# Performance work log

Hardware: AMD Instinct MI355X
Metric: run time of the kernel (lower is better)

## Reference

```python
import jax, jax.numpy as jnp
import numpy as np

EMB = 64
NODE_DIM = 5
T = 5
B, N = 8, 512


def setup_inputs() -> dict:
    key = jax.random.key(0)
    ks = jax.random.split(key, 24)
    def w(k, shape):
        return jax.random.normal(k, shape, dtype=jnp.float32) * 0.1
    xv = jax.random.normal(ks[0], (B, N, NODE_DIM), dtype=jnp.float32)
    Ws = jax.random.uniform(ks[1], (B, N, N), dtype=jnp.float32)
    reach = jax.random.bernoulli(ks[2], 0.5, (B, N))
    reach = reach.at[:, 0].set(True)  # guarantee at least one reachable node
    return {
        'xv': xv, 'Ws': Ws, 'reachable_nodes': reach,
        'W1a': w(ks[3], (NODE_DIM, EMB)), 'b1a': w(ks[4], (EMB,)),
        'W1b': w(ks[5], (EMB, EMB)),      'b1b': w(ks[6], (EMB,)),
        'W2':  w(ks[7], (EMB, EMB)),      'b2':  w(ks[8], (EMB,)),
        'W3':  w(ks[9], (EMB, EMB)),      'b3':  w(ks[10], (EMB,)),
        'w4':  w(ks[11], (EMB,)),         'b4':  w(ks[12], (EMB,)),
        'W6':  w(ks[13], (EMB, EMB)),     'b6':  w(ks[14], (EMB,)),
        'W7':  w(ks[15], (EMB, EMB)),     'b7':  w(ks[16], (EMB,)),
        'W51': w(ks[17], (2 * EMB, EMB)), 'b51': w(ks[18], (EMB,)),
        'w52': w(ks[19], (EMB,)),         'b52': w(ks[20], ()),
    }


def _struc2vec(xv, Ws, W1a, b1a, W1b, b1b, W2, b2, W3, b3, w4, b4):
    # s1: per-node feature embedding [B,N,E]
    s1 = jax.nn.relu(xv @ W1a + b1a) @ W1b + b1b
    # edge-feature path: relu(theta4(Ws[...,None])) summed over dim 1 -> [B,N,E]
    s3_1 = jax.nn.relu(Ws[..., None] * w4 + b4)  # [B,N,N,E]
    s3 = jnp.sum(s3_1, axis=1) @ W3 + b3         # [B,N,E]
    mu = jnp.zeros(s1.shape, dtype=s1.dtype)
    for _ in range(T):
        s2 = jnp.einsum('bnm,bme->bne', Ws, mu) @ W2 + b2
        mu = jax.nn.relu(s1 + s2 + s3)
    return mu


def reference(xv, Ws, reachable_nodes, W1a, b1a, W1b, b1b, W2, b2, W3, b3,
              w4, b4, W6, b6, W7, b7, W51, b51, w52, b52):
    mu = _struc2vec(xv, Ws, W1a, b1a, W1b, b1b, W2, b2, W3, b3, w4, b4)
    # global state broadcast to every node + local per-node action embedding
    global_state = jnp.sum(mu, axis=1, keepdims=True) @ W6 + b6  # [B,1,E]
    global_state = jnp.broadcast_to(global_state, mu.shape)      # [B,N,E]
    local_action = mu @ W7 + b7                                  # [B,N,E]
    rep = jax.nn.relu(jnp.concatenate([global_state, local_action], axis=2))
    rep = jax.nn.relu(rep) @ W51 + b51                           # relu(relu(.)) as in source
    prob_logits = rep @ w52 + b52                                # [B,N]
    prob_logits = jnp.where(reachable_nodes, prob_logits, -jnp.inf)
    return prob_logits
```

## Files before the change

### kernel.cpp

```cpp
#include <hip/hip_runtime.h>
#include <hip/hip_bf16.h>
#include <cstdint>
#include <cstddef>

#define BB 8
#define NN 512
#define EE 64

typedef __attribute__((ext_vector_type(8))) short short8v;
typedef __attribute__((ext_vector_type(4))) float f32x4;
typedef __attribute__((ext_vector_type(2))) float f32x2;
typedef __attribute__((ext_vector_type(4))) unsigned int u32x4;
typedef __attribute__((ext_vector_type(2))) unsigned int u32x2;

static __device__ __forceinline__ unsigned short f2bf(float f) {
  __hip_bfloat16 h = __float2bfloat16(f);
  return *reinterpret_cast<unsigned short*>(&h);
}
static __device__ __forceinline__ float bf2f(unsigned short u) {
  unsigned x = ((unsigned)u) << 16;
  float f; __builtin_memcpy(&f, &x, 4); return f;
}
static __device__ __forceinline__ u32x4 ld_b128_sc(const void* p) {
  u32x4 v;
  asm volatile("global_load_dwordx4 %0, %1, off sc0 sc1"
               : "=v"(v) : "v"(p) : "memory");
  return v;
}
static __device__ __forceinline__ unsigned ld_b32_sc(const void* p) {
  unsigned v;
  asm volatile("global_load_dword %0, %1, off sc0 sc1\n\ts_waitcnt vmcnt(0)"
               : "=v"(v) : "v"(p) : "memory");
  return v;
}
static __device__ __forceinline__ void st_b64_sc(void* p, u32x2 v) {
  asm volatile("global_store_dwordx2 %0, %1, off sc0 sc1"
               :: "v"(p), "v"(v) : "memory");
}
static __device__ __forceinline__ void st_b32_sc(void* p, unsigned v) {
  asm volatile("global_store_dword %0, %1, off sc0 sc1"
               :: "v"(p), "v"(v) : "memory");
}
static __device__ __forceinline__ void vm0() {
  asm volatile("s_waitcnt vmcnt(0)" ::: "memory");
}

__global__ __launch_bounds__(512) void k_fused(
    const float* __restrict__ Ws, const float* __restrict__ xv,
    const float* __restrict__ W1a, const float* __restrict__ b1a,
    const float* __restrict__ W1b, const float* __restrict__ b1b,
    const float* __restrict__ W2, const float* __restrict__ b2,
    const float* __restrict__ W3, const float* __restrict__ b3,
    const float* __restrict__ w4, const float* __restrict__ b4,
    const float* __restrict__ W6, const float* __restrict__ b6,
    const float* __restrict__ W7, const float* __restrict__ b7,
    const float* __restrict__ W51, const float* __restrict__ b51,
    const float* __restrict__ w52, const float* __restrict__ b52,
    const void* __restrict__ reach, float* __restrict__ out,
    unsigned short* __restrict__ z0, unsigned short* __restrict__ z1,
    unsigned short* __restrict__ z2, unsigned short* __restrict__ z3,
    float* __restrict__ gpart, unsigned* __restrict__ flags) {
  const int blk = blockIdx.x;
  const int b = (blk >> 3) & 7;
  const int stripe = ((blk & 7) << 2) | (blk >> 6);
  const int n0 = stripe << 4;
  const int t = threadIdx.x;
  const int w = t >> 6, l = t & 63, lr = l & 15, hi = l >> 4;
  const int lk = hi * 8, nq = hi * 4, eb = w & 3, kh = w >> 2;

  __shared__ __attribute__((aligned(16))) float tileT[16][132];
  __shared__ float sp[16][68];
  __shared__ float half_[16][68];
  __shared__ float hh[16][68];
  __shared__ float base_lds[16][68];
  __shared__ float yred[16][68];
  __shared__ __attribute__((aligned(16))) unsigned short muzA[512];
  __shared__ __attribute__((aligned(16))) unsigned short muzB[512];
  __shared__ float gsl[64], gsr[64], v7l[64], w52l[64], pl_lds[16];
  __shared__ float g0c;
  __shared__ int sbig, sflt;

  auto arrive = [&](int idx) {
    vm0();
    __syncthreads();
    if (t == 0) st_b32_sc(&flags[(b * 8 + idx) * 32 + stripe], 1u);
  };
  auto wait = [&](int idx) {
    if (t < 64) {
      const unsigned* fp = &flags[(b * 8 + idx) * 32 + (t & 31)];
      while (true) {
        unsigned v = ld_b32_sc(fp);
        if (__ballot(v != 0u) == ~0ull) break;
        __builtin_amdgcn_s_sleep(1);
      }
    }
    __syncthreads();
  };

  auto muz_store = [&](int node, int e, float v) {
    int eh = e & 31;
    unsigned short* dst = (e < 32) ? muzA : muzB;
    dst[((eh >> 3) * 16 + node) * 8 + (eh & 7)] = f2bf(v);
  };

  const float* wsbase = Ws + (size_t)b * NN * NN;
  const int lrow = t >> 2, lc4 = (t & 3) * 4;
  float4 tr0 = *(const float4*)&wsbase[(size_t)(0 * 128 + lrow) * NN + n0 + lc4];
  float4 tr1 = *(const float4*)&wsbase[(size_t)(1 * 128 + lrow) * NN + n0 + lc4];
  float4 tr2 = *(const float4*)&wsbase[(size_t)(2 * 128 + lrow) * NN + n0 + lc4];
  float4 tr3 = *(const float4*)&wsbase[(size_t)(3 * 128 + lrow) * NN + n0 + lc4];

  short8v WBa = {}, WBb = {};
  if (w < 4) {
    union { unsigned short u[8]; short8v v; } pa, pb;
#pragma unroll
    for (int j = 0; j < 8; ++j) {
      pa.u[j] = f2bf(W2[(8 * hi + j) * EE + 16 * w + lr]);
      pb.u[j] = f2bf(W2[(8 * hi + j + 32) * EE + 16 * w + lr]);
    }
    WBa = pa.v; WBb = pb.v;
  }

  {
    int e = t & 63;
#pragma unroll
    for (int p = 0; p < 2; ++p) {
      int rr = p * 8 + (t >> 6);
      const float* x = xv + ((size_t)b * NN + n0 + rr) * 5;
      float h = b1a[e];
      h = fmaf(x[0], W1a[0 * EE + e], h);
      h = fmaf(x[1], W1a[1 * EE + e], h);
      h = fmaf(x[2], W1a[2 * EE + e], h);
      h = fmaf(x[3], W1a[3 * EE + e], h);
      h = fmaf(x[4], W1a[4 * EE + e], h);
      hh[rr][e] = fmaxf(h, 0.f);
    }
  }
  {
    int ih = t >> 8;
    int n = (t >> 4) & 15;
    int e0 = (t & 15) * 4;
    float4 w4v = *(const float4*)&w4[e0];
    float4 b4v = *(const float4*)&b4[e0];
    f32x2 w4lo = {w4v.x, w4v.y}, w4hi_ = {w4v.z, w4v.w};
    f32x2 b4lo = {b4v.x, b4v.y}, b4hi_ = {b4v.z, b4v.w};
    f32x2 acclo = {0.f, 0.f}, acchi = {0.f, 0.f};
    const f32x2 zz = {0.f, 0.f};
    int ib = ih * 64;
#pragma unroll
    for (int c = 0; c < 4; ++c) {
      float4 tv = (c == 0) ? tr0 : (c == 1) ? tr1 : (c == 2) ? tr2 : tr3;
      tileT[lc4 + 0][lrow] = tv.x;
      tileT[lc4 + 1][lrow] = tv.y;
      tileT[lc4 + 2][lrow] = tv.z;
      tileT[lc4 + 3][lrow] = tv.w;
      __syncthreads();
#pragma unroll
      for (int i4 = 0; i4 < 16; ++i4) {
        float4 wv = *(const float4*)&tileT[n][ib + i4 * 4];
#pragma unroll
        for (int k = 0; k < 4; ++k) {
          float ww = (k == 0) ? wv.x : (k == 1) ? wv.y : (k == 2) ? wv.z : wv.w;
          f32x2 wp = {ww, ww};
          acclo += __builtin_elementwise_max(
              __builtin_elementwise_fma(wp, w4lo, b4lo), zz);
          acchi += __builtin_elementwise_max(
              __builtin_elementwise_fma(wp, w4hi_, b4hi_), zz);
        }
      }
      __syncthreads();
    }
    if (ih) {
      half_[n][e0] = acclo.x; half_[n][e0 + 1] = acclo.y;
      half_[n][e0 + 2] = acchi.x; half_[n][e0 + 3] = acchi.y;
    }
    __syncthreads();
    if (!ih) {
      sp[n][e0]     = acclo.x + half_[n][e0];
      sp[n][e0 + 1] = acclo.y + half_[n][e0 + 1];
      sp[n][e0 + 2] = acchi.x + half_[n][e0 + 2];
      sp[n][e0 + 3] = acchi.y + half_[n][e0 + 3];
    }
  }
  __syncthreads();
  {
    int e = t & 63;
#pragma unroll
    for (int p = 0; p < 2; ++p) {
      int rr = p * 8 + (t >> 6);
      float s = b1b[e] + b3[e] + b2[e];
#pragma unroll 8
      for (int j = 0; j < EE; ++j)
        s = fmaf(hh[rr][j], W1b[j * EE + e], fmaf(sp[rr][j], W3[j * EE + e], s));
      base_lds[rr][e] = s;
      muz_store(rr, e, fmaxf(s, 0.f));
    }
  }
  __syncthreads();

  auto zphase = [&](unsigned short* dst) {
    if (w < 4) {
      short8v a0 = *(const short8v*)&muzA[l * 8];
      short8v a1 = *(const short8v*)&muzB[l * 8];
      f32x4 zacc = {0.f, 0.f, 0.f, 0.f};
      zacc = __builtin_amdgcn_mfma_f32_16x16x32_bf16(a0, WBa, zacc, 0, 0, 0);
      zacc = __builtin_amdgcn_mfma_f32_16x16x32_bf16(a1, WBb, zacc, 0, 0, 0);
      ushort4 u;
      u.x = f2bf(zacc[0]); u.y = f2bf(zacc[1]);
      u.z = f2bf(zacc[2]); u.w = f2bf(zacc[3]);
      u32x2 v; __builtin_memcpy(&v, &u, 8);
      st_b64_sc(dst + ((size_t)b * EE + 16 * w + lr) * NN + n0 + 4 * hi, v);
    }
  };

  zphase(z0);
  arrive(0);

  short8v A0, A1, A2, A3, A4, A5, A6, A7;
  {
    const float* arow = wsbase + (size_t)(n0 + lr) * NN + kh * 256 + lk;
    union { unsigned short u[8]; short8v v; } pk;
#define LDA(DST, OFF)                                                        \
    { float4 fa = *(const float4*)(arow + OFF);                              \
      float4 fb = *(const float4*)(arow + OFF + 4);                          \
      pk.u[0] = f2bf(fa.x); pk.u[1] = f2bf(fa.y);                            \
      pk.u[2] = f2bf(fa.z); pk.u[3] = f2bf(fa.w);                            \
      pk.u[4] = f2bf(fb.x); pk.u[5] = f2bf(fb.y);                            \
      pk.u[6] = f2bf(fb.z); pk.u[7] = f2bf(fb.w);                            \
      DST = pk.v; }
    LDA(A0, 0)   LDA(A1, 32)  LDA(A2, 64)  LDA(A3, 96)
    LDA(A4, 128) LDA(A5, 160) LDA(A6, 192) LDA(A7, 224)
#undef LDA
  }

  auto prop = [&](const unsigned short* zsrc) {
    const unsigned short* Bp =
        zsrc + ((size_t)b * EE + eb * 16 + lr) * NN + kh * 256 + lk;
    short8v q0 = *(const short8v*)(Bp + 0);
    short8v q1 = *(const short8v*)(Bp + 32);
    short8v q2 = *(const short8v*)(Bp + 64);
    short8v q3 = *(const short8v*)(Bp + 96);
    short8v q4 = *(const short8v*)(Bp + 128);
    short8v q5 = *(const short8v*)(Bp + 160);
    short8v q6 = *(const short8v*)(Bp + 192);
    short8v q7 = *(const short8v*)(Bp + 224);
    f32x4 acc = {0.f, 0.f, 0.f, 0.f};
    acc = __builtin_amdgcn_mfma_f32_16x16x32_bf16(A0, q0, acc, 0, 0, 0);
    acc = __builtin_amdgcn_mfma_f32_16x16x32_bf16(A1, q1, acc, 0, 0, 0);
    acc = __builtin_amdgcn_mfma_f32_16x16x32_bf16(A2, q2, acc, 0, 0, 0);
    acc = __builtin_amdgcn_mfma_f32_16x16x32_bf16(A3, q3, acc, 0, 0, 0);
    acc = __builtin_amdgcn_mfma_f32_16x16x32_bf16(A4, q4, acc, 0, 0, 0);
    acc = __builtin_amdgcn_mfma_f32_16x16x32_bf16(A5, q5, acc, 0, 0, 0);
    acc = __builtin_amdgcn_mfma_f32_16x16x32_bf16(A6, q6, acc, 0, 0, 0);
    acc = __builtin_amdgcn_mfma_f32_16x16x32_bf16(A7, q7, acc, 0, 0, 0);
    if (kh == 1) {
#pragma unroll
      for (int q = 0; q < 4; ++q) yred[nq + q][eb * 16 + lr] = acc[q];
    }
    __syncthreads();
    if (kh == 0) {
      int ep = eb * 16 + lr;
#pragma unroll
      for (int q = 0; q < 4; ++q) {
        float v = fmaxf(base_lds[nq + q][ep] + acc[q] + yred[nq + q][ep], 0.f);
        muz_store(nq + q, ep, v);
      }
    }
    __syncthreads();
  };

  wait(0);
  prop(z0); zphase(z1); arrive(1); wait(1);
  prop(z1); zphase(z2); arrive(2); wait(2);
  prop(z2); zphase(z3); arrive(3); wait(3);
  prop(z3);

  if (t < 64) {
    int eh = t & 31, jj = t & 7, lb = (eh >> 3) * 16;
    const unsigned short* dst = (t < 32) ? muzA : muzB;
    float s = 0.f;
#pragma unroll
    for (int n = 0; n < 16; ++n) s += bf2f(dst[(lb + n) * 8 + jj]);
    st_b32_sc(&gpart[((size_t)b * 32 + stripe) * EE + t], __float_as_uint(s));
  }
  arrive(4);

  if (t == 0) { sbig = 0; sflt = 0; }
  if (t < 64) w52l[t] = w52[t];
  __syncthreads();
  if (t < 256) {
    const unsigned int* rw = (const unsigned int*)reach;
    bool big = false, flt = false;
#pragma unroll
    for (int l2 = 0; l2 < 4; ++l2) {
      unsigned int v = rw[t + l2 * 256];
      if (v > 1u) big = true;
      if (v == 0x3f800000u) flt = true;
    }
    if (big) sbig = 1;
    if (flt) sflt = 1;
  }
  if (t >= 320 && t < 384) {
    int j = t - 320;
    float v = 0.f;
#pragma unroll 8
    for (int e = 0; e < EE; ++e) v = fmaf(W51[(EE + j) * EE + e], w52[e], v);
    v7l[j] = v;
  }
  __syncthreads();
#pragma unroll
  for (int p = 0; p < 2; ++p) {
    int n = p * 8 + (t >> 6), e7 = t & 63;
    float la = b7[e7];
#pragma unroll
    for (int h = 0; h < 2; ++h) {
      const unsigned short* dst = h ? muzB : muzA;
#pragma unroll
      for (int h2 = 0; h2 < 4; ++h2) {
        short8v mv = *(const short8v*)&dst[(h2 * 16 + n) * 8];
#pragma unroll
        for (int j = 0; j < 8; ++j)
          la = fmaf(bf2f((unsigned short)mv[j]),
                    W7[(h * 32 + h2 * 8 + j) * EE + e7], la);
      }
    }
    float c = fmaxf(la, 0.f) * v7l[e7];
#pragma unroll
    for (int off = 32; off > 0; off >>= 1) c += __shfl_down(c, off, 64);
    if (e7 == 0) pl_lds[n] = c;
  }

  wait(4);

  float* gacc = &tileT[0][0];
  {
    int s = t >> 4, e4 = (t & 15) * 4;
    u32x4 v = ld_b128_sc(&gpart[((size_t)b * 32 + s) * EE + e4]);
    vm0();
    gacc[s * EE + e4 + 0] = __uint_as_float(v.x);
    gacc[s * EE + e4 + 1] = __uint_as_float(v.y);
    gacc[s * EE + e4 + 2] = __uint_as_float(v.z);
    gacc[s * EE + e4 + 3] = __uint_as_float(v.w);
  }
  __syncthreads();
  if (t < 64) {
    float s = 0.f;
#pragma unroll 8
    for (int k = 0; k < 32; ++k) s += gacc[k * EE + t];
    gsl[t] = s;
  }
  __syncthreads();
  if (t < 64) {
    float a = b6[t];
#pragma unroll 8
    for (int k = 0; k < EE; ++k) a = fmaf(gsl[k], W6[k * EE + t], a);
    gsr[t] = fmaxf(a, 0.f);
  }
  __syncthreads();
  if (t < 64) {
    float q = 0.f;
#pragma unroll 8
    for (int j = 0; j < EE; ++j) q = fmaf(gsr[j], W51[j * EE + t], q);
    float pg = (q + b51[t]) * w52l[t];
#pragma unroll
    for (int off = 32; off > 0; off >>= 1) pg += __shfl_down(pg, off, 64);
    if (t == 0) g0c = pg + b52[0];
  }
  __syncthreads();
  if (t < 16) {
    int row = b * NN + n0 + t;
    bool rc;
    if (sflt)      rc = ((const float*)reach)[row] != 0.f;
    else if (sbig) rc = ((const unsigned char*)reach)[row] != 0;
    else           rc = ((const int*)reach)[row] != 0;
    out[row] = rc ? (pl_lds[t] + g0c) : -1.0e30f;
  }
}

extern "C" void kernel_launch(void* const* d_in, const int* in_sizes, int n_in,
                              void* d_out, int out_size, void* d_ws, size_t ws_size,
                              hipStream_t stream) {
  const float* xv  = (const float*)d_in[0];
  const float* Ws  = (const float*)d_in[1];
  const void*  rch = d_in[2];
  const float* W1a = (const float*)d_in[3];
  const float* b1a = (const float*)d_in[4];
  const float* W1b = (const float*)d_in[5];
  const float* b1b = (const float*)d_in[6];
  const float* W2  = (const float*)d_in[7];
  const float* b2  = (const float*)d_in[8];
  const float* W3  = (const float*)d_in[9];
  const float* b3  = (const float*)d_in[10];
  const float* w4  = (const float*)d_in[11];
  const float* b4  = (const float*)d_in[12];
  const float* W6  = (const float*)d_in[13];
  const float* b6  = (const float*)d_in[14];
  const float* W7  = (const float*)d_in[15];
  const float* b7  = (const float*)d_in[16];
  const float* W51 = (const float*)d_in[17];
  const float* b51 = (const float*)d_in[18];
  const float* w52 = (const float*)d_in[19];
  const float* b52 = (const float*)d_in[20];
  float* out = (float*)d_out;

  char* wsb = (char*)d_ws;
  unsigned short* z0   = (unsigned short*)wsb;
  unsigned short* z1   = (unsigned short*)(wsb + (512 << 10));
  unsigned short* z2   = (unsigned short*)(wsb + (1024 << 10));
  unsigned short* z3   = (unsigned short*)(wsb + (1536 << 10));
  float* gpart         = (float*)(wsb + (2048 << 10));
  unsigned* flags      = (unsigned*)(wsb + (2112 << 10));

  hipMemsetAsync((void*)flags, 0, 8192, stream);
  k_fused<<<dim3(256), dim3(512), 0, stream>>>(
      Ws, xv, W1a, b1a, W1b, b1b, W2, b2, W3, b3, w4, b4,
      W6, b6, W7, b7, W51, b51, w52, b52, rch, out,
      z0, z1, z2, z3, gpart, flags);
}
```

Baseline: 57.13 us.

## Replace global barrier waits with per-stripe flag polling in propagation

Instead of waiting for all blocks of a batch to arrive before each propagation step, each wave polls per-stripe flags and issues MFMAs for k-chunks whose producer stripes have finished, accumulating as data becomes available. This is meant to overlap the cross-block dependency wait with compute and remove the full-barrier stall. It adds polling loops with s_sleep and ballot, and relies on flag semantics matching the arrive() layout, which is not shown.

```diff
diff --git a/kernel.cpp b/kernel.cpp
--- a/kernel.cpp
+++ b/kernel.cpp
@@ -216,64 +216,69 @@
   zphase(z0);
   arrive(0);
 
-  short8v A0, A1, A2, A3, A4, A5, A6, A7;
+  short8v Afr[8];
   {
     const float* arow = wsbase + (size_t)(n0 + lr) * NN + kh * 256 + lk;
     union { unsigned short u[8]; short8v v; } pk;
-#define LDA(DST, OFF)                                                        \
-    { float4 fa = *(const float4*)(arow + OFF);                              \
-      float4 fb = *(const float4*)(arow + OFF + 4);                          \
-      pk.u[0] = f2bf(fa.x); pk.u[1] = f2bf(fa.y);                            \
-      pk.u[2] = f2bf(fa.z); pk.u[3] = f2bf(fa.w);                            \
-      pk.u[4] = f2bf(fb.x); pk.u[5] = f2bf(fb.y);                            \
-      pk.u[6] = f2bf(fb.z); pk.u[7] = f2bf(fb.w);                            \
-      DST = pk.v; }
-    LDA(A0, 0)   LDA(A1, 32)  LDA(A2, 64)  LDA(A3, 96)
-    LDA(A4, 128) LDA(A5, 160) LDA(A6, 192) LDA(A7, 224)
-#undef LDA
-  }
-
-  auto prop = [&](const unsigned short* zsrc) {
+#pragma unroll
+    for (int j = 0; j < 8; ++j) {
+      float4 fa = *(const float4*)(arow + 32 * j);
+      float4 fb = *(const float4*)(arow + 32 * j + 4);
+      pk.u[0] = f2bf(fa.x); pk.u[1] = f2bf(fa.y);
+      pk.u[2] = f2bf(fa.z); pk.u[3] = f2bf(fa.w);
+      pk.u[4] = f2bf(fb.x); pk.u[5] = f2bf(fb.y);
+      pk.u[6] = f2bf(fb.z); pk.u[7] = f2bf(fb.w);
+      Afr[j] = pk.v;
+    }
+  }
+
+  auto prop = [&](const unsigned short* zsrc, int idx) {
+    const unsigned* fb = &flags[(b * 8 + idx) * 32];
     const unsigned short* Bp =
         zsrc + ((size_t)b * EE + eb * 16 + lr) * NN + kh * 256 + lk;
-    short8v q0 = *(const short8v*)(Bp + 0);
-    short8v q1 = *(const short8v*)(Bp + 32);
-    short8v q2 = *(const short8v*)(Bp + 64);
-    short8v q3 = *(const short8v*)(Bp + 96);
-    short8v q4 = *(const short8v*)(Bp + 128);
-    short8v q5 = *(const short8v*)(Bp + 160);
-    short8v q6 = *(const short8v*)(Bp + 192);
-    short8v q7 = *(const short8v*)(Bp + 224);
     f32x4 acc = {0.f, 0.f, 0.f, 0.f};
-    acc = __builtin_amdgcn_mfma_f32_16x16x32_bf16(A0, q0, acc, 0, 0, 0);
-    acc = __builtin_amdgcn_mfma_f32_16x16x32_bf16(A1, q1, acc, 0, 0, 0);
-    acc = __builtin_amdgcn_mfma_f32_16x16x32_bf16(A2, q2, acc, 0, 0, 0);
-    acc = __builtin_amdgcn_mfma_f32_16x16x32_bf16(A3, q3, acc, 0, 0, 0);
-    acc = __builtin_amdgcn_mfma_f32_16x16x32_bf16(A4, q4, acc, 0, 0, 0);
-    acc = __builtin_amdgcn_mfma_f32_16x16x32_bf16(A5, q5, acc, 0, 0, 0);
-    acc = __builtin_amdgcn_mfma_f32_16x16x32_bf16(A6, q6, acc, 0, 0, 0);
-    acc = __builtin_amdgcn_mfma_f32_16x16x32_bf16(A7, q7, acc, 0, 0, 0);
+    unsigned done = 0;
+    while (done != 0xFFu) {
+      unsigned fv = (l < 32) ? ld_b32_sc(fb + l) : 0u;
+      unsigned long long bm = __ballot(fv != 0u);
+      unsigned m32 = (unsigned)bm;
+      unsigned pr = m32 & (m32 >> 1);
+      short8v q[8];
+      unsigned newly = 0;
+#pragma unroll
+      for (int j = 0; j < 8; ++j) {
+        if (!(done & (1u << j)) && ((pr >> (16 * kh + 2 * j)) & 1u)) {
+          q[j] = *(const short8v*)(Bp + 32 * j);
+          newly |= 1u << j;
+        }
+      }
+#pragma unroll
+      for (int j = 0; j < 8; ++j)
+        if (newly & (1u << j))
+          acc = __builtin_amdgcn_mfma_f32_16x16x32_bf16(Afr[j], q[j], acc, 0, 0, 0);
+      done |= newly;
+      if (done != 0xFFu) __builtin_amdgcn_s_sleep(1);
+    }
     if (kh == 1) {
 #pragma unroll
-      for (int q = 0; q < 4; ++q) yred[nq + q][eb * 16 + lr] = acc[q];
+      for (int q2 = 0; q2 < 4; ++q2) yred[nq + q2][eb * 16 + lr] = acc[q2];
     }
     __syncthreads();
     if (kh == 0) {
       int ep = eb * 16 + lr;
 #pragma unroll
-      for (int q = 0; q < 4; ++q) {
-        float v = fmaxf(base_lds[nq + q][ep] + acc[q] + yred[nq + q][ep], 0.f);
-        muz_store(nq + q, ep, v);
+      for (int q2 = 0; q2 < 4; ++q2) {
+        float v = fmaxf(base_lds[nq + q2][ep] + acc[q2] + yred[nq + q2][ep], 0.f);
+        muz_store(nq + q2, ep, v);
       }
     }
     __syncthreads();
   };
 
-  wait(0);
-  prop(z0); zphase(z1); arrive(1); wait(1);
-  prop(z1); zphase(z2); arrive(2); wait(2);
-  prop(z2); zphase(z3); arrive(3); wait(3);
-  prop(z3);
+  prop(z0, 0); zphase(z1); arrive(1);
+  prop(z1, 1); zphase(z2); arrive(2);
+  prop(z2, 2); zphase(z3); arrive(3);
+  prop(z3, 3);
 
   if (t < 64) {
     int eh = t & 31, jj = t & 7, lb = (eh >> 3) * 16;
```

Result: slower. 58.37 us (+2.2%).
